# Performance work log

Hardware: AMD Instinct MI355X
Metric: run time of the kernel (lower is better)

The kernel has to match this reference:

```python
import jax, jax.numpy as jnp
import numpy as np

N_EMBD = 1024
N_HEAD = 16
HEAD = N_EMBD // N_HEAD


def setup_inputs() -> dict:
    key = jax.random.key(0)
    ks = jax.random.split(key, 5)
    B, T = 2, 2048
    s = 1.0 / np.sqrt(N_EMBD)
    return {
        "x": jax.random.normal(ks[0], (B, T, N_EMBD), jnp.float32),
        "w_attn": jax.random.normal(ks[1], (N_EMBD, 3 * N_EMBD), jnp.float32) * s,
        "b_attn": jnp.zeros((3 * N_EMBD,), jnp.float32),
        "w_proj": jax.random.normal(ks[2], (N_EMBD, N_EMBD), jnp.float32) * s,
        "b_proj": jnp.zeros((N_EMBD,), jnp.float32),
    }


def reference(x, w_attn, b_attn, w_proj, b_proj):
    B, T, C = x.shape
    qkv = x @ w_attn + b_attn                      # [B,T,3C]
    q, k, v = jnp.split(qkv, 3, axis=-1)
    def heads(t):
        return t.reshape(B, T, N_HEAD, HEAD).transpose(0, 2, 1, 3)  # [B,H,T,D]
    q, k, v = heads(q), heads(k), heads(v)
    scale = 1.0 / np.sqrt(HEAD)
    att = jnp.einsum('bhqd,bhkd->bhqk', q, k) * scale
    causal = jnp.tril(jnp.ones((T, T), bool))
    att = jnp.where(causal, att, -jnp.inf)
    p = jax.nn.softmax(att, axis=-1)
    y = jnp.einsum('bhqk,bhkd->bhqd', p, v)        # [B,H,T,D]
    y = y.transpose(0, 2, 1, 3).reshape(B, T, C)
    return y @ w_proj + b_proj
```

## Files before the change

kernel.cpp:

```cpp
#include <hip/hip_runtime.h>
#include <hip/hip_bf16.h>

typedef __attribute__((ext_vector_type(4))) float f32x4;
typedef __attribute__((ext_vector_type(16))) float f32x16;
typedef __attribute__((ext_vector_type(8))) short bf16x8;
typedef __attribute__((ext_vector_type(4))) unsigned int u32x4;

#define MFMA16(a,b,c) __builtin_amdgcn_mfma_f32_16x16x32_bf16(a,b,c,0,0,0)
#define MFMA32(a,b,c) __builtin_amdgcn_mfma_f32_32x32x16_bf16(a,b,c,0,0,0)
#define LOG2E 1.44269504088896340736f

__device__ __forceinline__ float bf2f(unsigned short u){
  unsigned v = ((unsigned)u) << 16;
  float f; __builtin_memcpy(&f, &v, 4); return f;
}
__device__ __forceinline__ unsigned short f2bf(float f){
  unsigned x; __builtin_memcpy(&x, &f, 4);
  x += 0x7fffu + ((x >> 16) & 1u);
  return (unsigned short)(x >> 16);
}
__device__ __forceinline__ void gload_lds16(const void* g, void* l){
  __builtin_amdgcn_global_load_lds((const __attribute__((address_space(1))) void*)g,
                                   (__attribute__((address_space(3))) void*)l, 16, 0, 0);
}
__device__ __forceinline__ f32x16 zero16(){
  f32x16 z;
#pragma unroll
  for (int i = 0; i < 16; ++i) z[i] = 0.f;
  return z;
}
__device__ __forceinline__ unsigned cvtpk(float lo, float hi_){
  unsigned d;
  asm("v_cvt_pk_bf16_f32 %0, %1, %2" : "=v"(d) : "v"(lo), "v"(hi_));
  return d;
}
__device__ __forceinline__ void pack_group(const float* p, bf16x8& f0, bf16x8& f1){
  unsigned a0 = cvtpk(p[0], p[1]),  b0 = cvtpk(p[4],  p[5]);
  unsigned a1 = cvtpk(p[2], p[3]),  b1 = cvtpk(p[6],  p[7]);
  unsigned c0 = cvtpk(p[8], p[9]),  d0 = cvtpk(p[12], p[13]);
  unsigned c1 = cvtpk(p[10],p[11]), d1 = cvtpk(p[14], p[15]);
  asm("v_permlane32_swap_b32 %0, %1" : "+v"(a0), "+v"(b0));
  asm("v_permlane32_swap_b32 %0, %1" : "+v"(a1), "+v"(b1));
  asm("v_permlane32_swap_b32 %0, %1" : "+v"(c0), "+v"(d0));
  asm("v_permlane32_swap_b32 %0, %1" : "+v"(c1), "+v"(d1));
  u32x4 w0 = {a0, a1, b0, b1};
  u32x4 w1 = {c0, c1, d0, d1};
  f0 = __builtin_bit_cast(bf16x8, w0);
  f1 = __builtin_bit_cast(bf16x8, w1);
}

__global__ void k_cast(const float* __restrict__ src, unsigned short* __restrict__ dst){
  const int i = blockIdx.x * 256 + threadIdx.x;
  const float4 v = ((const float4*)src)[i];
  ushort4 o;
  o.x = f2bf(v.x); o.y = f2bf(v.y); o.z = f2bf(v.z); o.w = f2bf(v.w);
  ((ushort4*)dst)[i] = o;
}

__global__ void k_castT(const float* __restrict__ src, unsigned short* __restrict__ dst,
                        const int R, const int C){
  __shared__ unsigned short t[64][65];
  const int r0 = blockIdx.y * 64, c0 = blockIdx.x * 64;
  const int tid = threadIdx.x;
#pragma unroll
  for (int i = 0; i < 16; ++i){
    int idx = i*256 + tid; int r = idx >> 6, c = idx & 63;
    t[r][c] = f2bf(src[(size_t)(r0 + r)*C + c0 + c]);
  }
  __syncthreads();
#pragma unroll
  for (int i = 0; i < 16; ++i){
    int idx = i*256 + tid; int c = idx >> 6, r = idx & 63;
    dst[(size_t)(c0 + c)*R + r0 + r] = t[r][c];
  }
}

__device__ __forceinline__ void gemm_core(const unsigned short* __restrict__ A,
                                          const unsigned short* __restrict__ Bt,
                                          const int K, const int bm, const int bn,
                                          unsigned short* lds, f32x4 acc[4][4])
{
  const int tid  = threadIdx.x;
  const int lane = tid & 63;
  const int wave = tid >> 6;
  const int wr = wave >> 1, wc = wave & 1;
  const int l15 = lane & 15, lg = lane >> 4;
  char* ldsb = (char*)lds;
  const int aoff = (wr*64 + l15)*64 + lg*16;
  const int boff = 8192 + (wc*64 + l15)*64 + lg*16;
  const int o0 = wave*1024 + lane*16;
  const int o1 = o0 + 4096;
  const int r0_ = o0 >> 6, c0_ = (o0 & 63) >> 1;
  const int r1_ = o1 >> 6, c1_ = (o1 & 63) >> 1;
  const unsigned short* Ap0 = A  + (size_t)(bm + r0_)*K + c0_;
  const unsigned short* Ap1 = A  + (size_t)(bm + r1_)*K + c1_;
  const unsigned short* Bp0 = Bt + (size_t)(bn + r0_)*K + c0_;
  const unsigned short* Bp1 = Bt + (size_t)(bn + r1_)*K + c1_;
  char* dA0 = ldsb + wave*1024;
  char* dA1 = ldsb + 4096 + wave*1024;
  char* dB0 = ldsb + 8192 + wave*1024;
  char* dB1 = ldsb + 12288 + wave*1024;
  for (int k0 = 0; k0 < K; k0 += 32){
    __syncthreads();
    gload_lds16(Ap0 + k0, dA0);
    gload_lds16(Ap1 + k0, dA1);
    gload_lds16(Bp0 + k0, dB0);
    gload_lds16(Bp1 + k0, dB1);
    __syncthreads();
    bf16x8 af[4], bg[4];
#pragma unroll
    for (int m = 0; m < 4; ++m) af[m] = *(const bf16x8*)(ldsb + aoff + m*1024);
#pragma unroll
    for (int n = 0; n < 4; ++n) bg[n] = *(const bf16x8*)(ldsb + boff + n*1024);
#pragma unroll
    for (int m = 0; m < 4; ++m)
#pragma unroll
      for (int n = 0; n < 4; ++n)
        acc[m][n] = MFMA16(af[m], bg[n], acc[m][n]);
  }
}

__global__ __launch_bounds__(256,2) void k_gemm_qkv(const unsigned short* __restrict__ xb,
    const unsigned short* __restrict__ waT, const float* __restrict__ b_attn,
    unsigned short* __restrict__ qb, unsigned short* __restrict__ kb,
    unsigned short* __restrict__ vb)
{
  __shared__ unsigned short lds[8192];
  f32x4 acc[4][4];
#pragma unroll
  for (int m = 0; m < 4; ++m)
#pragma unroll
    for (int n = 0; n < 4; ++n) acc[m][n] = (f32x4){0.f,0.f,0.f,0.f};
  int wgid = blockIdx.y * gridDim.x + blockIdx.x;
  const int cpx = (gridDim.x * gridDim.y) >> 3;
  wgid = (wgid & 7) * cpx + (wgid >> 3);
  const int bm = (wgid / gridDim.x) * 128, bn = (wgid % gridDim.x) * 128;
  gemm_core(xb, waT, 1024, bm, bn, lds, acc);
  const int lane = threadIdx.x & 63, wave = threadIdx.x >> 6;
  const int wr = wave >> 1, wc = wave & 1, l15 = lane & 15, lg = lane >> 4;
#pragma unroll
  for (int m = 0; m < 4; ++m){
#pragma unroll
    for (int n = 0; n < 4; ++n){
#pragma unroll
      for (int r = 0; r < 4; ++r){
        const int row = bm + wr*64 + m*16 + lg*4 + r;
        const int col = bn + wc*64 + n*16 + l15;
        const float val = acc[m][n][r] + b_attn[col];
        const int part = col >> 10, c = col & 1023;
        const int h = c >> 6, d = c & 63;
        const int b = row >> 11, t = row & 2047;
        const unsigned short u = f2bf(val);
        const size_t bhbase = (size_t)(b*16 + h)*131072;
        if (part == 0){
          qb[bhbase + (size_t)t*64 + d] = u;
        } else {
          const int tile = t >> 6, l = t & 63;
          const size_t base = bhbase + (size_t)tile*4096;
          if (part == 1) kb[base + l*64 + ((((d>>3)^(l&7))<<3) | (d&7))] = u;
          else           vb[base + d*64 + ((((l>>3)^(d&7))<<3) | (l&7))] = u;
        }
      }
    }
  }
}

__global__ __launch_bounds__(256,2) void k_gemm_proj(const unsigned short* __restrict__ yb,
    const unsigned short* __restrict__ wpT, const float* __restrict__ b_proj,
    float* __restrict__ out)
{
  __shared__ unsigned short lds[8192];
  f32x4 acc[4][4];
#pragma unroll
  for (int m = 0; m < 4; ++m)
#pragma unroll
    for (int n = 0; n < 4; ++n) acc[m][n] = (f32x4){0.f,0.f,0.f,0.f};
  int wgid = blockIdx.y * gridDim.x + blockIdx.x;
  const int cpx = (gridDim.x * gridDim.y) >> 3;
  wgid = (wgid & 7) * cpx + (wgid >> 3);
  const int bm = (wgid / gridDim.x) * 128, bn = (wgid % gridDim.x) * 128;
  gemm_core(yb, wpT, 1024, bm, bn, lds, acc);
  const int lane = threadIdx.x & 63, wave = threadIdx.x >> 6;
  const int wr = wave >> 1, wc = wave & 1, l15 = lane & 15, lg = lane >> 4;
#pragma unroll
  for (int m = 0; m < 4; ++m){
#pragma unroll
    for (int n = 0; n < 4; ++n){
#pragma unroll
      for (int r = 0; r < 4; ++r){
        const int row = bm + wr*64 + m*16 + lg*4 + r;
        const int col = bn + wc*64 + n*16 + l15;
        out[(size_t)row*1024 + col] = acc[m][n][r] + b_proj[col];
      }
    }
  }
}

__global__ __launch_bounds__(256,2) void k_attn(const unsigned short* __restrict__ q,
                       const unsigned short* __restrict__ kt,
                       const unsigned short* __restrict__ vt,
                       unsigned short* __restrict__ y)
{
  __shared__ char lds[32768];
  const int tid = threadIdx.x, lane = tid & 63, wave = tid >> 6;
  const int l31 = lane & 31, hi = lane >> 5;
  const int i = blockIdx.x, ii = i & 255;
  const int bh = ii & 31;
  const int qbi = (i < 256) ? (15 - (ii >> 5)) : (ii >> 5);
  const int q0w = qbi*128 + wave*32;
  const int ntiles = (qbi + 1) * 2;
  const unsigned short* qh = q + (size_t)bh * 131072;
  const char* kbase = (const char*)(kt + (size_t)bh * 131072);
  const char* vbase = (const char*)(vt + (size_t)bh * 131072);

  const float C = 0.125f * LOG2E;
  const float M = 16.0f;

  bf16x8 qf[4];
  {
    const unsigned short* qp = qh + (size_t)(q0w + l31)*64 + hi*8;
#pragma unroll
    for (int ds = 0; ds < 4; ++ds) qf[ds] = *(const bf16x8*)(qp + ds*16);
  }

  f32x16 yac0 = zero16(), yac1 = zero16();
  float lsum = 0.f;
  const int mask_from = q0w >> 6;
  const int stg = tid * 16;
  const int dst = wave * 1024;
  char* ldsK = lds;
  char* ldsV = lds + 16384;

#define STAGE(tile, buf) do { \
    const char* ks_ = kbase + (size_t)(tile)*8192; \
    const char* vs_ = vbase + (size_t)(tile)*8192; \
    gload_lds16(ks_ + stg,        ldsK + (buf)*8192 + dst); \
    gload_lds16(ks_ + 4096 + stg, ldsK + (buf)*8192 + 4096 + dst); \
    gload_lds16(vs_ + stg,        ldsV + (buf)*8192 + dst); \
    gload_lds16(vs_ + 4096 + stg, ldsV + (buf)*8192 + 4096 + dst); \
  } while(0)

  STAGE(0, 0);
  __syncthreads();

  const int swz = (l31 & 7) << 4;
  const int rowb = l31 * 128;

  for (int t = 0; t < ntiles; ++t){
    const int buf = t & 1;
    if (t + 1 < ntiles) STAGE(t + 1, buf ^ 1);

    const char* kb_ = ldsK + buf*8192;
    const char* vb_ = ldsV + buf*8192;

    bf16x8 kf[8];
#pragma unroll
    for (int ds = 0; ds < 4; ++ds){
      const int ch = ((ds*2 + hi) << 4) ^ swz;
      kf[ds]   = *(const bf16x8*)(kb_ + rowb + ch);
      kf[ds+4] = *(const bf16x8*)(kb_ + 4096 + rowb + ch);
    }
    f32x16 s0 = zero16(), s1 = zero16();
#pragma unroll
    for (int ds = 0; ds < 4; ++ds){
      s0 = MFMA32(kf[ds],   qf[ds], s0);
      s1 = MFMA32(kf[ds+4], qf[ds], s1);
    }

    bf16x8 vf[8];
#pragma unroll
    for (int ks = 0; ks < 4; ++ks){
      const int ch = ((ks*2 + hi) << 4) ^ swz;
      vf[ks]   = *(const bf16x8*)(vb_ + rowb + ch);
      vf[ks+4] = *(const bf16x8*)(vb_ + 4096 + rowb + ch);
    }

    if (t >= mask_from){
      const int qg = q0w + l31, key0 = t << 6;
#pragma unroll
      for (int r = 0; r < 16; ++r){
        const int kl = (r&3) + 8*(r>>2) + 4*hi;
        if (key0 + kl      > qg) s0[r] = -1e30f;
        if (key0 + 32 + kl > qg) s1[r] = -1e30f;
      }
    }

    float p0[16], p1[16];
    float ts = 0.f;
#pragma unroll
    for (int r = 0; r < 16; ++r){
      p0[r] = __builtin_amdgcn_exp2f(__builtin_fmaf(s0[r], C, -M));
      p1[r] = __builtin_amdgcn_exp2f(__builtin_fmaf(s1[r], C, -M));
      ts += p0[r] + p1[r];
    }
    lsum += ts;

    bf16x8 pa[4];
    pack_group(p0, pa[0], pa[1]);
    pack_group(p1, pa[2], pa[3]);
#pragma unroll
    for (int ks = 0; ks < 4; ++ks){
      yac0 = MFMA32(pa[ks], vf[ks],   yac0);
      yac1 = MFMA32(pa[ks], vf[ks+4], yac1);
    }
    __syncthreads();
  }
#undef STAGE

  lsum += __shfl_xor(lsum, 32);
  const float linv = 1.0f / lsum;
  const int b = bh >> 4, h = bh & 15;
  unsigned short* yp = y + ((size_t)b*2048 + q0w)*1024 + h*64;
#pragma unroll
  for (int r = 0; r < 16; ++r){
    const int ql = (r&3) + 8*(r>>2) + 4*hi;
    const float li = __shfl(linv, ql);
    yp[(size_t)ql*1024 + l31]      = f2bf(yac0[r] * li);
    yp[(size_t)ql*1024 + 32 + l31] = f2bf(yac1[r] * li);
  }
}

extern "C" void kernel_launch(void* const* d_in, const int* in_sizes, int n_in,
                              void* d_out, int out_size, void* d_ws, size_t ws_size,
                              hipStream_t stream) {
  const float* x      = (const float*)d_in[0];
  const float* w_attn = (const float*)d_in[1];
  const float* b_attn = (const float*)d_in[2];
  const float* w_proj = (const float*)d_in[3];
  const float* b_proj = (const float*)d_in[4];
  float* out = (float*)d_out;

  unsigned short* ws  = (unsigned short*)d_ws;
  unsigned short* xb  = ws;
  unsigned short* waT = xb  + 4194304;
  unsigned short* wpT = waT + 3145728;
  unsigned short* qb  = wpT + 1048576;
  unsigned short* kb  = qb  + 4194304;
  unsigned short* vb  = kb  + 4194304;
  unsigned short* yb  = vb  + 4194304;

  k_cast<<<dim3(4096), dim3(256), 0, stream>>>(x, xb);
  k_castT<<<dim3(48,16), dim3(256), 0, stream>>>(w_attn, waT, 1024, 3072);
  k_castT<<<dim3(16,16), dim3(256), 0, stream>>>(w_proj, wpT, 1024, 1024);
  k_gemm_qkv<<<dim3(24,32), dim3(256), 0, stream>>>(xb, waT, b_attn, qb, kb, vb);
  k_attn<<<dim3(512), dim3(256), 0, stream>>>(qb, kb, vb, yb);
  k_gemm_proj<<<dim3(8,32), dim3(256), 0, stream>>>(yb, wpT, b_proj, out);
}
```

Before: 105.3 us.

## Rewrite QKV GEMM as 256x256 tile with 8 waves and double-buffered pipelined loads

Replaces the 128x128, 4-wave QKV GEMM with a 256x256 tile, 8-wave kernel that uses 128KB of double-buffered LDS with swizzled layout. Global-to-LDS loads for the next K step are staggered between MFMA phases, separated by barriers, and MFMA sections run at raised wave priority. The aim is to raise arithmetic intensity per tile and hide load latency behind compute. In exchange the grid shrinks to 192 workgroups, which may leave many CUs idle. The 128KB LDS footprint also likely limits occupancy to one workgroup per CU despite the launch bounds.

```diff
diff --git a/kernel.cpp b/kernel.cpp
--- a/kernel.cpp
+++ b/kernel.cpp
@@ -72,6 +72,125 @@
   for (int i = 0; i < 16; ++i){
     int idx = i*256 + tid; int c = idx >> 6, r = idx & 63;
     dst[(size_t)(c0 + c)*R + r0 + r] = t[r][c];
+  }
+}
+
+__global__ __launch_bounds__(512,2) void k_gemm_qkv(const unsigned short* __restrict__ xb,
+    const unsigned short* __restrict__ waT, const float* __restrict__ b_attn,
+    unsigned short* __restrict__ qb, unsigned short* __restrict__ kb,
+    unsigned short* __restrict__ vb)
+{
+  __shared__ char lds[131072];
+  const int K = 1024, NT = 16;
+  const int tid = threadIdx.x, lane = tid & 63, wave = tid >> 6;
+  const int wr = wave >> 2, wc = wave & 3;
+  const int l15 = lane & 15, lg = lane >> 4;
+
+  int wgid = blockIdx.y * 12 + blockIdx.x;
+  wgid = (wgid & 7) * 24 + (wgid >> 3);
+  const int bm = (wgid / 12) * 256, bn = (wgid % 12) * 256;
+
+  const int soff = wave*1024 + lane*16;
+  const int srow = soff >> 7;
+  const int schv = ((soff >> 4) & 7) ^ (srow & 7);
+  const unsigned short* gA = xb  + (size_t)(bm + srow)*K + schv*8;
+  const unsigned short* gB = waT + (size_t)(bn + srow)*K + schv*8;
+  const int ldst = wave*1024;
+  char* const ldsp = (char*)lds;
+
+  const int c0 = ((lg    ) ^ (l15 & 7)) * 16;
+  const int c1 = ((4 + lg) ^ (l15 & 7)) * 16;
+  const int laneA = l15 * 128;
+
+  f32x4 acc[8][4];
+#pragma unroll
+  for (int m = 0; m < 8; ++m)
+#pragma unroll
+    for (int n = 0; n < 4; ++n) acc[m][n] = (f32x4){0.f,0.f,0.f,0.f};
+
+#define STG(T, PR) do { if ((T) < NT) { \
+    const int b_ = (T) & 1; const int i0_ = ((PR) & 1) * 2; \
+    if ((PR) < 2) { \
+      gload_lds16(gA + (size_t)(i0_  )*64*1024 + (T)*64, ldsp + b_*65536 + (i0_  )*8192 + ldst); \
+      gload_lds16(gA + (size_t)(i0_+1)*64*1024 + (T)*64, ldsp + b_*65536 + (i0_+1)*8192 + ldst); \
+    } else { \
+      gload_lds16(gB + (size_t)(i0_  )*64*1024 + (T)*64, ldsp + b_*65536 + 32768 + (i0_  )*8192 + ldst); \
+      gload_lds16(gB + (size_t)(i0_+1)*64*1024 + (T)*64, ldsp + b_*65536 + 32768 + (i0_+1)*8192 + ldst); \
+    } } } while(0)
+
+#define LDA(MH) _Pragma("unroll") for (int m = 0; m < 4; ++m){ \
+    a[2*m]   = *(const bf16x8*)(Aw + (MH)*8192 + m*2048 + c0); \
+    a[2*m+1] = *(const bf16x8*)(Aw + (MH)*8192 + m*2048 + c1); }
+#define LDB(NH) _Pragma("unroll") for (int n = 0; n < 2; ++n){ \
+    b[2*((NH)*2+n)]   = *(const bf16x8*)(Bw + ((NH)*2+n)*2048 + c0); \
+    b[2*((NH)*2+n)+1] = *(const bf16x8*)(Bw + ((NH)*2+n)*2048 + c1); }
+#define P_MFMA(MH, NLO) \
+  __builtin_amdgcn_s_setprio(1); \
+  _Pragma("unroll") for (int m = 0; m < 4; ++m){ \
+    _Pragma("unroll") for (int n = 0; n < 2; ++n){ \
+      acc[(MH)*4+m][(NLO)+n] = MFMA16(a[2*m],   b[2*((NLO)+n)],   acc[(MH)*4+m][(NLO)+n]); \
+      acc[(MH)*4+m][(NLO)+n] = MFMA16(a[2*m+1], b[2*((NLO)+n)+1], acc[(MH)*4+m][(NLO)+n]); \
+    } } \
+  __builtin_amdgcn_s_setprio(0);
+#define WAIT_LGKM asm volatile("s_waitcnt lgkmcnt(0)" ::: "memory"); __builtin_amdgcn_sched_barrier(0);
+
+  STG(0,0); STG(0,1); STG(0,2); STG(0,3); STG(1,0);
+
+  bf16x8 a[8], b[8];
+  for (int t = 0; t < NT; ++t){
+    const char* Aw = ldsp + (t&1)*65536 + wr*16384 + laneA;
+    const char* Bw = ldsp + (t&1)*65536 + 32768 + wc*8192 + laneA;
+    asm volatile("s_waitcnt vmcnt(2)" ::: "memory");
+    __builtin_amdgcn_s_barrier();
+    LDA(0); LDB(0);
+    STG(t+1, 1);
+    __builtin_amdgcn_s_barrier();
+    WAIT_LGKM;
+    P_MFMA(0, 0);
+    LDB(1);
+    STG(t+1, 2);
+    __builtin_amdgcn_s_barrier();
+    WAIT_LGKM;
+    P_MFMA(0, 2);
+    LDA(1);
+    STG(t+1, 3);
+    __builtin_amdgcn_s_barrier();
+    WAIT_LGKM;
+    P_MFMA(1, 2);
+    __builtin_amdgcn_s_barrier();
+    STG(t+2, 0);
+    P_MFMA(1, 0);
+  }
+#undef STG
+#undef LDA
+#undef LDB
+#undef P_MFMA
+#undef WAIT_LGKM
+
+#pragma unroll
+  for (int am = 0; am < 8; ++am){
+#pragma unroll
+    for (int an = 0; an < 4; ++an){
+#pragma unroll
+      for (int r = 0; r < 4; ++r){
+        const int row = bm + wr*128 + am*16 + lg*4 + r;
+        const int col = bn + wc*64 + an*16 + l15;
+        const float val = acc[am][an][r] + b_attn[col];
+        const int part = col >> 10, c = col & 1023;
+        const int h = c >> 6, d = c & 63;
+        const int bb = row >> 11, tt = row & 2047;
+        const unsigned short u = f2bf(val);
+        const size_t bhbase = (size_t)(bb*16 + h)*131072;
+        if (part == 0){
+          qb[bhbase + (size_t)tt*64 + d] = u;
+        } else {
+          const int tile = tt >> 6, l = tt & 63;
+          const size_t base = bhbase + (size_t)tile*4096;
+          if (part == 1) kb[base + l*64 + ((((d>>3)^(l&7))<<3) | (d&7))] = u;
+          else           vb[base + d*64 + ((((l>>3)^(d&7))<<3) | (l&7))] = u;
+        }
+      }
+    }
   }
 }
 
@@ -120,51 +239,6 @@
   }
 }
 
-__global__ __launch_bounds__(256,2) void k_gemm_qkv(const unsigned short* __restrict__ xb,
-    const unsigned short* __restrict__ waT, const float* __restrict__ b_attn,
-    unsigned short* __restrict__ qb, unsigned short* __restrict__ kb,
-    unsigned short* __restrict__ vb)
-{
-  __shared__ unsigned short lds[8192];
-  f32x4 acc[4][4];
-#pragma unroll
-  for (int m = 0; m < 4; ++m)
-#pragma unroll
-    for (int n = 0; n < 4; ++n) acc[m][n] = (f32x4){0.f,0.f,0.f,0.f};
-  int wgid = blockIdx.y * gridDim.x + blockIdx.x;
-  const int cpx = (gridDim.x * gridDim.y) >> 3;
-  wgid = (wgid & 7) * cpx + (wgid >> 3);
-  const int bm = (wgid / gridDim.x) * 128, bn = (wgid % gridDim.x) * 128;
-  gemm_core(xb, waT, 1024, bm, bn, lds, acc);
-  const int lane = threadIdx.x & 63, wave = threadIdx.x >> 6;
-  const int wr = wave >> 1, wc = wave & 1, l15 = lane & 15, lg = lane >> 4;
-#pragma unroll
-  for (int m = 0; m < 4; ++m){
-#pragma unroll
-    for (int n = 0; n < 4; ++n){
-#pragma unroll
-      for (int r = 0; r < 4; ++r){
-        const int row = bm + wr*64 + m*16 + lg*4 + r;
-        const int col = bn + wc*64 + n*16 + l15;
-        const float val = acc[m][n][r] + b_attn[col];
-        const int part = col >> 10, c = col & 1023;
-        const int h = c >> 6, d = c & 63;
-        const int b = row >> 11, t = row & 2047;
-        const unsigned short u = f2bf(val);
-        const size_t bhbase = (size_t)(b*16 + h)*131072;
-        if (part == 0){
-          qb[bhbase + (size_t)t*64 + d] = u;
-        } else {
-          const int tile = t >> 6, l = t & 63;
-          const size_t base = bhbase + (size_t)tile*4096;
-          if (part == 1) kb[base + l*64 + ((((d>>3)^(l&7))<<3) | (d&7))] = u;
-          else           vb[base + d*64 + ((((l>>3)^(d&7))<<3) | (l&7))] = u;
-        }
-      }
-    }
-  }
-}
-
 __global__ __launch_bounds__(256,2) void k_gemm_proj(const unsigned short* __restrict__ yb,
     const unsigned short* __restrict__ wpT, const float* __restrict__ b_proj,
     float* __restrict__ out)
@@ -342,7 +416,7 @@
   k_cast<<<dim3(4096), dim3(256), 0, stream>>>(x, xb);
   k_castT<<<dim3(48,16), dim3(256), 0, stream>>>(w_attn, waT, 1024, 3072);
   k_castT<<<dim3(16,16), dim3(256), 0, stream>>>(w_proj, wpT, 1024, 1024);
-  k_gemm_qkv<<<dim3(24,32), dim3(256), 0, stream>>>(xb, waT, b_attn, qb, kb, vb);
+  k_gemm_qkv<<<dim3(12,16), dim3(512), 0, stream>>>(xb, waT, b_attn, qb, kb, vb);
   k_attn<<<dim3(512), dim3(256), 0, stream>>>(qb, kb, vb, yb);
   k_gemm_proj<<<dim3(8,32), dim3(256), 0, stream>>>(yb, wpT, b_proj, out);
 }
```

New measurement: 108.6 us. +3.2%, slower.

## Triple-buffer GEMM LDS staging with swizzled layout and async prefetch

Applied to the files above, without the earlier changes.

Replaces the single-buffered GEMM main loop (two barriers per k-step, loads then compute) with a three-stage LDS ring. Tiles are prefetched two steps ahead using global_load_lds, and synchronisation uses vmcnt waits plus one barrier per step. It also XOR-swizzles the LDS column chunks to reduce bank conflicts, and raises MFMA priority around the compute block. The LDS footprint triples to 48KB, launch bounds change to 3 waves/EU, and the grid swizzle is hard-coded to the fixed problem sizes.

```diff
diff --git a/kernel.cpp b/kernel.cpp
--- a/kernel.cpp
+++ b/kernel.cpp
@@ -75,67 +75,74 @@
   }
 }
 
-__device__ __forceinline__ void gemm_core(const unsigned short* __restrict__ A,
-                                          const unsigned short* __restrict__ Bt,
-                                          const int K, const int bm, const int bn,
-                                          unsigned short* lds, f32x4 acc[4][4])
+__device__ __forceinline__ void gemm_core3(const unsigned short* __restrict__ A,
+                                           const unsigned short* __restrict__ Bt,
+                                           const int K, const int bm, const int bn,
+                                           char* ldsb, f32x4 acc[4][4])
 {
-  const int tid  = threadIdx.x;
-  const int lane = tid & 63;
-  const int wave = tid >> 6;
+  const int tid = threadIdx.x, lane = tid & 63, wave = tid >> 6;
   const int wr = wave >> 1, wc = wave & 1;
   const int l15 = lane & 15, lg = lane >> 4;
-  char* ldsb = (char*)lds;
-  const int aoff = (wr*64 + l15)*64 + lg*16;
-  const int boff = 8192 + (wc*64 + l15)*64 + lg*16;
-  const int o0 = wave*1024 + lane*16;
-  const int o1 = o0 + 4096;
-  const int r0_ = o0 >> 6, c0_ = (o0 & 63) >> 1;
-  const int r1_ = o1 >> 6, c1_ = (o1 & 63) >> 1;
-  const unsigned short* Ap0 = A  + (size_t)(bm + r0_)*K + c0_;
-  const unsigned short* Ap1 = A  + (size_t)(bm + r1_)*K + c1_;
-  const unsigned short* Bp0 = Bt + (size_t)(bn + r0_)*K + c0_;
-  const unsigned short* Bp1 = Bt + (size_t)(bn + r1_)*K + c1_;
-  char* dA0 = ldsb + wave*1024;
-  char* dA1 = ldsb + 4096 + wave*1024;
-  char* dB0 = ldsb + 8192 + wave*1024;
-  char* dB1 = ldsb + 12288 + wave*1024;
-  for (int k0 = 0; k0 < K; k0 += 32){
-    __syncthreads();
-    gload_lds16(Ap0 + k0, dA0);
-    gload_lds16(Ap1 + k0, dA1);
-    gload_lds16(Bp0 + k0, dB0);
-    gload_lds16(Bp1 + k0, dB1);
-    __syncthreads();
+  const int o = tid * 16;
+  const int srow = o >> 6;
+  const int sch = ((o >> 4) & 3) ^ ((srow >> 1) & 3);
+  const unsigned short* gA0 = A  + (size_t)(bm + srow)*K      + sch*8;
+  const unsigned short* gA1 = A  + (size_t)(bm + 64 + srow)*K + sch*8;
+  const unsigned short* gB0 = Bt + (size_t)(bn + srow)*K      + sch*8;
+  const unsigned short* gB1 = Bt + (size_t)(bn + 64 + srow)*K + sch*8;
+  const int rsw = (l15 >> 1) & 3;
+  const int aoff = (wr*64 + l15)*64 + ((lg ^ rsw) << 4);
+  const int boff = 8192 + (wc*64 + l15)*64 + ((lg ^ rsw) << 4);
+
+#define STG3(koff, bb) do { \
+    gload_lds16(gA0 + (koff), ldsb + (bb) + o); \
+    gload_lds16(gA1 + (koff), ldsb + (bb) + 4096 + o); \
+    gload_lds16(gB0 + (koff), ldsb + (bb) + 8192 + o); \
+    gload_lds16(gB1 + (koff), ldsb + (bb) + 12288 + o); } while(0)
+
+  const int NT = K >> 5;
+  STG3(0, 0);
+  STG3(32, 16384);
+  int bcur = 0, bstg = 32768;
+  for (int t = 0; t < NT; ++t){
+    if (t + 1 < NT) asm volatile("s_waitcnt vmcnt(4)" ::: "memory");
+    else            asm volatile("s_waitcnt vmcnt(0)" ::: "memory");
+    __builtin_amdgcn_s_barrier();
+    __builtin_amdgcn_sched_barrier(0);
+    if (t + 2 < NT) STG3((size_t)(t + 2) << 5, bstg);
     bf16x8 af[4], bg[4];
 #pragma unroll
-    for (int m = 0; m < 4; ++m) af[m] = *(const bf16x8*)(ldsb + aoff + m*1024);
-#pragma unroll
-    for (int n = 0; n < 4; ++n) bg[n] = *(const bf16x8*)(ldsb + boff + n*1024);
+    for (int m = 0; m < 4; ++m) af[m] = *(const bf16x8*)(ldsb + bcur + aoff + m*1024);
+#pragma unroll
+    for (int n = 0; n < 4; ++n) bg[n] = *(const bf16x8*)(ldsb + bcur + boff + n*1024);
+    __builtin_amdgcn_s_setprio(1);
 #pragma unroll
     for (int m = 0; m < 4; ++m)
 #pragma unroll
       for (int n = 0; n < 4; ++n)
         acc[m][n] = MFMA16(af[m], bg[n], acc[m][n]);
-  }
-}
-
-__global__ __launch_bounds__(256,2) void k_gemm_qkv(const unsigned short* __restrict__ xb,
+    __builtin_amdgcn_s_setprio(0);
+    bcur = (bcur == 32768) ? 0 : bcur + 16384;
+    bstg = (bstg == 32768) ? 0 : bstg + 16384;
+  }
+#undef STG3
+}
+
+__global__ __launch_bounds__(256,3) void k_gemm_qkv(const unsigned short* __restrict__ xb,
     const unsigned short* __restrict__ waT, const float* __restrict__ b_attn,
     unsigned short* __restrict__ qb, unsigned short* __restrict__ kb,
     unsigned short* __restrict__ vb)
 {
-  __shared__ unsigned short lds[8192];
+  __shared__ char lds[49152];
   f32x4 acc[4][4];
 #pragma unroll
   for (int m = 0; m < 4; ++m)
 #pragma unroll
     for (int n = 0; n < 4; ++n) acc[m][n] = (f32x4){0.f,0.f,0.f,0.f};
-  int wgid = blockIdx.y * gridDim.x + blockIdx.x;
-  const int cpx = (gridDim.x * gridDim.y) >> 3;
-  wgid = (wgid & 7) * cpx + (wgid >> 3);
-  const int bm = (wgid / gridDim.x) * 128, bn = (wgid % gridDim.x) * 128;
-  gemm_core(xb, waT, 1024, bm, bn, lds, acc);
+  int wgid = blockIdx.y * 24 + blockIdx.x;
+  wgid = (wgid & 7) * 96 + (wgid >> 3);
+  const int bm = (wgid / 24) * 128, bn = (wgid % 24) * 128;
+  gemm_core3(xb, waT, 1024, bm, bn, lds, acc);
   const int lane = threadIdx.x & 63, wave = threadIdx.x >> 6;
   const int wr = wave >> 1, wc = wave & 1, l15 = lane & 15, lg = lane >> 4;
 #pragma unroll
@@ -165,21 +172,20 @@
   }
 }
 
-__global__ __launch_bounds__(256,2) void k_gemm_proj(const unsigned short* __restrict__ yb,
+__global__ __launch_bounds__(256,3) void k_gemm_proj(const unsigned short* __restrict__ yb,
     const unsigned short* __restrict__ wpT, const float* __restrict__ b_proj,
     float* __restrict__ out)
 {
-  __shared__ unsigned short lds[8192];
+  __shared__ char lds[49152];
   f32x4 acc[4][4];
 #pragma unroll
   for (int m = 0; m < 4; ++m)
 #pragma unroll
     for (int n = 0; n < 4; ++n) acc[m][n] = (f32x4){0.f,0.f,0.f,0.f};
-  int wgid = blockIdx.y * gridDim.x + blockIdx.x;
-  const int cpx = (gridDim.x * gridDim.y) >> 3;
-  wgid = (wgid & 7) * cpx + (wgid >> 3);
-  const int bm = (wgid / gridDim.x) * 128, bn = (wgid % gridDim.x) * 128;
-  gemm_core(yb, wpT, 1024, bm, bn, lds, acc);
+  int wgid = blockIdx.y * 8 + blockIdx.x;
+  wgid = (wgid & 7) * 32 + (wgid >> 3);
+  const int bm = (wgid / 8) * 128, bn = (wgid % 8) * 128;
+  gemm_core3(yb, wpT, 1024, bm, bn, lds, acc);
   const int lane = threadIdx.x & 63, wave = threadIdx.x >> 6;
   const int wr = wave >> 1, wc = wave & 1, l15 = lane & 15, lg = lane >> 4;
 #pragma unroll
```

Result: faster. 101.0 us (-4.1%).
